# Optimization experiments

Measured on AMD Instinct MI355X. Metric: run time of the kernel, lower is better.

The kernel has to match this reference:

```python
import jax, jax.numpy as jnp
import numpy as np

N, E, H, NF, EF = 50000, 1600000, 128, 8, 2


def setup_inputs() -> dict:
    key = jax.random.key(0)
    ks = jax.random.split(key, 24)
    rn = lambda k, shp, s=0.05: jax.random.normal(k, shp, jnp.float32) * s
    inp = {
        "x": jax.random.normal(ks[0], (N, NF), jnp.float32),
        "edge_index": jax.random.randint(ks[1], (2, E), 0, N),
        "edge_attr": jax.random.normal(ks[2], (E, EF), jnp.float32),
        "enc_W": rn(ks[3], (NF, H)),
        "enc_b": jnp.zeros((H,), jnp.float32),
        "bn_g": jnp.ones((H,), jnp.float32),
        "bn_b": jnp.zeros((H,), jnp.float32),
    }
    i = 4
    for l in (1, 2, 3):
        inp[f"W{l}"] = rn(ks[i], (H, H))
        inp[f"asrc{l}"] = rn(ks[i + 1], (H,))
        inp[f"adst{l}"] = rn(ks[i + 2], (H,))
        inp[f"We{l}"] = rn(ks[i + 3], (EF, H))
        inp[f"ae{l}"] = rn(ks[i + 4], (H,))
        inp[f"b{l}"] = jnp.zeros((H,), jnp.float32)
        i += 5
    return inp


def _gat(h, src, dst, ea, W, a_s, a_d, We, a_e, b, n):
    # PyG GATConv, heads=1, concat=True, negative_slope=0.2
    g = h @ W                                   # [N, H] transformed nodes
    a_src = g @ a_s                             # [N] per-source attention term
    a_dst = g @ a_d                             # [N] per-target attention term
    a_edge = (ea @ We) @ a_e                    # [E'] edge-conditioned term
    logit = jax.nn.leaky_relu(a_src[src] + a_dst[dst] + a_edge, negative_slope=0.2)
    # scatter-softmax over incoming edges of each destination node
    m = jax.ops.segment_max(logit, dst, num_segments=n)
    e = jnp.exp(logit - m[dst])
    s = jax.ops.segment_sum(e, dst, num_segments=n)
    alpha = e / (s[dst] + 1e-16)                # [E']
    out = jax.ops.segment_sum(g[src] * alpha[:, None], dst, num_segments=n)
    return out + b


def _forward(x, edge_index, edge_attr, enc_W, enc_b, bn_g, bn_b,
             W1, asrc1, adst1, We1, ae1, b1,
             W2, asrc2, adst2, We2, ae2, b2,
             W3, asrc3, adst3, We3, ae3, b3):
    n = x.shape[0]
    # PyG add_self_loops=True with fill_value='mean' for edge_attr
    loop = jnp.arange(n)
    src = jnp.concatenate([edge_index[0], loop])
    dst = jnp.concatenate([edge_index[1], loop])
    ea = jnp.concatenate([edge_attr, jnp.broadcast_to(edge_attr.mean(0), (n, edge_attr.shape[1]))], axis=0)
    # node encoder: Linear -> BatchNorm1d (eval: running_mean=0, running_var=1) -> ReLU (dropout off)
    inv = np.float32(1.0 / np.sqrt(1.0 + 1e-5))
    h0 = jax.nn.relu((x @ enc_W + enc_b) * (bn_g * inv) + bn_b)
    h1 = jax.nn.relu(_gat(h0, src, dst, ea, W1, asrc1, adst1, We1, ae1, b1, n))
    h2 = jax.nn.relu(_gat(h1, src, dst, ea, W2, asrc2, adst2, We2, ae2, b2, n))
    h3 = _gat(h2, src, dst, ea, W3, asrc3, adst3, We3, ae3, b3, n)
    return h3 + h0


def reference(x, edge_index, edge_attr, enc_W, enc_b, bn_g, bn_b,
              W1, asrc1, adst1, We1, ae1, b1,
              W2, asrc2, adst2, We2, ae2, b2,
              W3, asrc3, adst3, We3, ae3, b3):
    return _forward(x, edge_index, edge_attr, enc_W, enc_b, bn_g, bn_b,
                    W1, asrc1, adst1, We1, ae1, b1,
                    W2, asrc2, adst2, We2, ae2, b2,
                    W3, asrc3, adst3, We3, ae3, b3)
```

## Files before the change

### kernel.cpp

```cpp
#include <hip/hip_runtime.h>
#include <math.h>


#define H 128
#define NF 8
#define EPB 4096

typedef __attribute__((ext_vector_type(8))) short short8v;
typedef __attribute__((ext_vector_type(4))) float f32x4;

__device__ __forceinline__ float wred_sum(float x) {
#pragma unroll
    for (int m = 32; m >= 1; m >>= 1) x += __shfl_xor(x, m, 64);
    return x;
}
__device__ __forceinline__ float wred_max(float x) {
#pragma unroll
    for (int m = 32; m >= 1; m >>= 1) x = fmaxf(x, __shfl_xor(x, m, 64));
    return x;
}
__device__ __forceinline__ ushort f2bf(float f) {
    uint u = __float_as_uint(f);
    uint r = (u + 0x7FFFu + ((u >> 16) & 1u)) >> 16;
    return (ushort)r;
}


__global__ void k_count(const int* __restrict__ ei, const float* __restrict__ ea,
                        int E, int nblk, int nbuckets, int* __restrict__ bucketTotal,
                        int* __restrict__ blockBase, float2* __restrict__ pmean) {
    __shared__ int hist[256];
    __shared__ float sx[4], sy[4];
    int t = threadIdx.x;
    int blk = blockIdx.x;
    hist[t] = 0;
    __syncthreads();
    int base = blk * EPB;
    float px = 0.f, py = 0.f;
#pragma unroll
    for (int i = 0; i < 16; ++i) {
        int e = base + i * 256 + t;
        if (e < E) {
            int d = ei[E + e];
            atomicAdd(&hist[d >> 8], 1);
            const float2 z = *(const float2*)(ea + 2 * (size_t)e);
            px += z.x; py += z.y;
        }
    }
    px = wred_sum(px); py = wred_sum(py);
    if ((t & 63) == 0) { sx[t >> 6] = px; sy[t >> 6] = py; }
    __syncthreads();
    if (t == 0) {
        pmean[blk] = make_float2(sx[0] + sx[1] + sx[2] + sx[3],
                                 sy[0] + sy[1] + sy[2] + sy[3]);
    }
    if (t < nbuckets) {
        int c = hist[t];
        int old = (c > 0) ? atomicAdd(&bucketTotal[t], c) : 0;
        blockBase[t * nblk + blk] = old;
    }
}

__global__ void k_scan_park(const int* __restrict__ bucketTotal, int nbuckets,
                            int* __restrict__ bucketBase, int* __restrict__ rowptr,
                            int N, int E, const float2* __restrict__ pmean, int nblk,
                            float invE,
                            const float* __restrict__ We1, const float* __restrict__ ae1,
                            const float* __restrict__ We2, const float* __restrict__ ae2,
                            const float* __restrict__ We3, const float* __restrict__ ae3,
                            float* __restrict__ park) {
    __shared__ int tmp[256];
    __shared__ float2 sp[4];
    __shared__ float smean[2];
    int t = threadIdx.x;
    float ax = 0.f, ay = 0.f;
    for (int i = t; i < nblk; i += 256) {
        float2 z = pmean[i];
        ax += z.x; ay += z.y;
    }
    ax = wred_sum(ax); ay = wred_sum(ay);
    if ((t & 63) == 0) sp[t >> 6] = make_float2(ax, ay);
    int v = (t < nbuckets) ? bucketTotal[t] : 0;
    tmp[t] = v;
    __syncthreads();
    for (int off = 1; off < 256; off <<= 1) {
        int q = (t >= off) ? tmp[t - off] : 0;
        __syncthreads();
        tmp[t] += q;
        __syncthreads();
    }
    bucketBase[t] = tmp[t] - v;
    if (t == 0) {
        bucketBase[256] = tmp[255];
        rowptr[N] = E;
        smean[0] = (sp[0].x + sp[1].x + sp[2].x + sp[3].x) * invE;
        smean[1] = (sp[0].y + sp[1].y + sp[2].y + sp[3].y) * invE;
    }
    __syncthreads();
    if (t < 192) {
        int l = t >> 6, q = t & 63;
        const float* We = (l == 0) ? We1 : ((l == 1) ? We2 : We3);
        const float* ae = (l == 0) ? ae1 : ((l == 1) ? ae2 : ae3);
        float p0 = We[q] * ae[q] + We[q + 64] * ae[q + 64];
        float p1 = We[H + q] * ae[q] + We[H + q + 64] * ae[q + 64];
        p0 = wred_sum(p0);
        p1 = wred_sum(p1);
        if (q == 0) {
            park[l * 3 + 0] = p0;
            park[l * 3 + 1] = p1;
            park[l * 3 + 2] = smean[0] * p0 + smean[1] * p1;
        }
    }
}

__global__ void k_place(const int* __restrict__ ei, const float* __restrict__ ea,
                        int E, int nblk, int nbuckets,
                        const int* __restrict__ bucketBase, const int* __restrict__ blockBase,
                        uint2* __restrict__ temp) {
    __shared__ int cnt[256];
    __shared__ int sbase[256];
    int t = threadIdx.x;
    int blk = blockIdx.x;
    cnt[t] = 0;
    if (t < nbuckets) sbase[t] = bucketBase[t] + blockBase[t * nblk + blk];
    __syncthreads();
    int base = blk * EPB;
#pragma unroll
    for (int i = 0; i < 16; ++i) {
        int e = base + i * 256 + t;
        if (e < E) {
            int s = ei[e];
            int d = ei[E + e];
            int b = d >> 8;
            int r = atomicAdd(&cnt[b], 1);
            const float2 z = *(const float2*)(ea + 2 * (size_t)e);
            uint w0 = (uint)s | ((uint)(d & 255) << 16);
            uint w1 = (uint)f2bf(z.x) | ((uint)f2bf(z.y) << 16);
            temp[sbase[b] + r] = make_uint2(w0, w1);
        }
    }
}

__global__ void k_fine(const uint2* __restrict__ temp, const int* __restrict__ bucketBase,
                       const float* __restrict__ park, int N,
                       uint* __restrict__ er0, uint* __restrict__ er1,
                       uint* __restrict__ er2, int* __restrict__ rowptr) {
    __shared__ int hist[256];
    __shared__ int tmp[256];
    __shared__ int fb[256];
    __shared__ int cur[256];
    int b = blockIdx.x;
    int t = threadIdx.x;
    const int lo = bucketBase[b], hi = bucketBase[b + 1];
    hist[t] = 0;
    __syncthreads();
    for (int e = lo + t; e < hi; e += 256) {
        atomicAdd(&hist[(temp[e].x >> 16) & 255], 1);
    }
    __syncthreads();
    int v = hist[t];
    tmp[t] = v;
    __syncthreads();
    for (int off = 1; off < 256; off <<= 1) {
        int q = (t >= off) ? tmp[t - off] : 0;
        __syncthreads();
        tmp[t] += q;
        __syncthreads();
    }
    fb[t] = tmp[t] - v;
    cur[t] = 0;
    int dst = b * 256 + t;
    if (dst < N) rowptr[dst] = lo + fb[t];
    __syncthreads();
    const float c00 = park[0], c01 = park[1];
    const float c10 = park[3], c11 = park[4];
    const float c20 = park[6], c21 = park[7];
    for (int e = lo + t; e < hi; e += 256) {
        uint2 w = temp[e];
        uint src = w.x & 0xFFFFu;
        int j = (int)((w.x >> 16) & 255u);
        float ex = __uint_as_float(w.y << 16);
        float ey = __uint_as_float(w.y & 0xffff0000u);
        int r = atomicAdd(&cur[j], 1);
        int p = lo + fb[j] + r;
        er0[p] = src | ((uint)f2bf(c00 * ex + c01 * ey) << 16);
        er1[p] = src | ((uint)f2bf(c10 * ex + c11 * ey) << 16);
        er2[p] = src | ((uint)f2bf(c20 * ex + c21 * ey) << 16);
    }
}

__global__ void k_wpack(const float* __restrict__ W1, const float* __restrict__ W2,
                        const float* __restrict__ W3, ushort* __restrict__ Wp) {
    int layer = blockIdx.x;
    const float* W = (layer == 0) ? W1 : ((layer == 1) ? W2 : W3);
    for (int idx = threadIdx.x; idx < 16384; idx += 256) {
        int i = idx & 7;
        int lane = (idx >> 3) & 63;
        int ft = idx >> 9;
        int kt = ft & 3, nt = ft >> 2;
        int k = kt * 32 + (lane >> 4) * 8 + i;
        int n = nt * 16 + (lane & 15);
        Wp[layer * 16384 + idx] = f2bf(W[k * H + n]);
    }
}

__global__ void k_encoder(const float* __restrict__ x, const float* __restrict__ encW,
                          const float* __restrict__ encb, const float* __restrict__ bng,
                          const float* __restrict__ bnb, float* __restrict__ h0,
                          ushort* __restrict__ hb, int N) {
    __shared__ float xs[8 * NF];
    int tid = threadIdx.x;
    int nb = blockIdx.x * 8;
    if (tid < 64) {
        size_t idx = (size_t)nb * NF + tid;
        xs[tid] = (idx < (size_t)N * NF) ? x[idx] : 0.f;
    }
    __syncthreads();
    int jt = tid & 31, i = tid >> 5;
    int node = nb + i;
    int j4 = jt * 4;
    float ax = 0.f, ay = 0.f, az = 0.f, aw = 0.f;
#pragma unroll
    for (int k = 0; k < NF; ++k) {
        float hx = xs[i * NF + k];
        const float4 w = *(const float4*)(encW + k * H + j4);
        ax = fmaf(hx, w.x, ax); ay = fmaf(hx, w.y, ay);
        az = fmaf(hx, w.z, az); aw = fmaf(hx, w.w, aw);
    }
    if (node < N) {
        const float inv = 0.9999950000374997f;
        const float4 eb = *(const float4*)(encb + j4);
        const float4 gg = *(const float4*)(bng + j4);
        const float4 bb = *(const float4*)(bnb + j4);
        float4 o;
        o.x = fmaxf(0.f, (ax + eb.x) * (gg.x * inv) + bb.x);
        o.y = fmaxf(0.f, (ay + eb.y) * (gg.y * inv) + bb.y);
        o.z = fmaxf(0.f, (az + eb.z) * (gg.z * inv) + bb.z);
        o.w = fmaxf(0.f, (aw + eb.w) * (gg.w * inv) + bb.w);
        *(float4*)(h0 + (size_t)node * H + j4) = o;
        uint2 ob;
        ob.x = (uint)f2bf(o.x) | ((uint)f2bf(o.y) << 16);
        ob.y = (uint)f2bf(o.z) | ((uint)f2bf(o.w) << 16);
        *(uint2*)(hb + (size_t)node * H + j4) = ob;
    }
}

__global__ void k_gemm_mfma(const ushort* __restrict__ hb, const ushort* __restrict__ Wp,
                            const float* __restrict__ avs, const float* __restrict__ avd,
                            ushort* __restrict__ gb, float* __restrict__ a_src,
                            float* __restrict__ a_dst, int N) {
    __shared__ ushort hs[64 * 136];
    int tid = threadIdx.x;
    int nb = blockIdx.x * 64;
#pragma unroll
    for (int it = 0; it < 4; ++it) {
        int fi = it * 256 + tid;
        int r = fi >> 4;
        int c8 = (fi & 15) * 8;
        int node = nb + r;
        uint4 v = make_uint4(0, 0, 0, 0);
        if (node < N) v = *(const uint4*)(hb + (size_t)node * H + c8);
        *(uint4*)(hs + r * 136 + c8) = v;
    }
    __syncthreads();
    const int l = tid & 63;
    const int w = tid >> 6;
    const int cl = l & 15;
    const int kg = l >> 4;
    const ushort* hrow = hs + (w * 16 + cl) * 136 + kg * 8;
    short8v a0 = *(const short8v*)(hrow + 0);
    short8v a1 = *(const short8v*)(hrow + 32);
    short8v a2 = *(const short8v*)(hrow + 64);
    short8v a3 = *(const short8v*)(hrow + 96);

    f32x4 acc[8];
#pragma unroll
    for (int nt = 0; nt < 8; ++nt) {
        const short8v* bp = (const short8v*)(Wp + ((size_t)(nt * 4) * 64 + l) * 8);
        f32x4 c = {0.f, 0.f, 0.f, 0.f};
        c = __builtin_amdgcn_mfma_f32_16x16x32_bf16(a0, bp[0], c, 0, 0, 0);
        c = __builtin_amdgcn_mfma_f32_16x16x32_bf16(a1, bp[64], c, 0, 0, 0);
        c = __builtin_amdgcn_mfma_f32_16x16x32_bf16(a2, bp[128], c, 0, 0, 0);
        c = __builtin_amdgcn_mfma_f32_16x16x32_bf16(a3, bp[192], c, 0, 0, 0);
        acc[nt] = c;
    }

    float ps0 = 0.f, ps1 = 0.f, ps2 = 0.f, ps3 = 0.f;
    float pd0 = 0.f, pd1 = 0.f, pd2 = 0.f, pd3 = 0.f;
#pragma unroll
    for (int nt = 0; nt < 8; ++nt) {
        float vs = avs[cl + 16 * nt];
        float vd = avd[cl + 16 * nt];
        ps0 = fmaf(acc[nt].x, vs, ps0); pd0 = fmaf(acc[nt].x, vd, pd0);
        ps1 = fmaf(acc[nt].y, vs, ps1); pd1 = fmaf(acc[nt].y, vd, pd1);
        ps2 = fmaf(acc[nt].z, vs, ps2); pd2 = fmaf(acc[nt].z, vd, pd2);
        ps3 = fmaf(acc[nt].w, vs, ps3); pd3 = fmaf(acc[nt].w, vd, pd3);
    }
#pragma unroll
    for (int m = 8; m >= 1; m >>= 1) {
        ps0 += __shfl_xor(ps0, m, 64); pd0 += __shfl_xor(pd0, m, 64);
        ps1 += __shfl_xor(ps1, m, 64); pd1 += __shfl_xor(pd1, m, 64);
        ps2 += __shfl_xor(ps2, m, 64); pd2 += __shfl_xor(pd2, m, 64);
        ps3 += __shfl_xor(ps3, m, 64); pd3 += __shfl_xor(pd3, m, 64);
    }
    int r0 = nb + w * 16 + kg * 4;
    if (cl == 0) {
        if (r0 + 0 < N) { a_src[r0 + 0] = ps0; a_dst[r0 + 0] = pd0; }
        if (r0 + 1 < N) { a_src[r0 + 1] = ps1; a_dst[r0 + 1] = pd1; }
        if (r0 + 2 < N) { a_src[r0 + 2] = ps2; a_dst[r0 + 2] = pd2; }
        if (r0 + 3 < N) { a_src[r0 + 3] = ps3; a_dst[r0 + 3] = pd3; }
    }
#pragma unroll
    for (int nt = 0; nt < 8; ++nt) {
        int col = nt * 16 + cl;
        if (r0 + 0 < N) gb[(size_t)(r0 + 0) * H + col] = f2bf(acc[nt].x);
        if (r0 + 1 < N) gb[(size_t)(r0 + 1) * H + col] = f2bf(acc[nt].y);
        if (r0 + 2 < N) gb[(size_t)(r0 + 2) * H + col] = f2bf(acc[nt].z);
        if (r0 + 3 < N) gb[(size_t)(r0 + 3) * H + col] = f2bf(acc[nt].w);
    }
}

template <int MODE>
__global__ void k_agg(const ushort* __restrict__ gb, const float* __restrict__ a_src,
                      const float* __restrict__ a_dst, const int* __restrict__ rowptr,
                      const uint* __restrict__ erecL, const float* __restrict__ park,
                      int layer, const float* __restrict__ bias,
                      const float* __restrict__ h0, float* __restrict__ outf,
                      ushort* __restrict__ outb, int N) {
    int wv = threadIdx.x >> 6;
    int lane = threadIdx.x & 63;
    int v = blockIdx.x * 4 + wv;
    if (v >= N) return;

    const int grp = lane >> 4;
    const int sub = lane & 15;
    const int ch8 = sub * 8;

    const float sa = park[layer * 3 + 2];
    const float adv = a_dst[v];
    float lself = a_src[v] + adv + sa;
    lself = (lself > 0.f) ? lself : 0.2f * lself;

    float m = lself;
    float s = 1.f;
    float acc[8];
    {
        const uint4 q = *(const uint4*)(gb + (size_t)v * H + ch8);
        float sel = (grp == 0) ? 1.f : 0.f;
        acc[0] = sel * __uint_as_float(q.x << 16);
        acc[1] = sel * __uint_as_float(q.x & 0xffff0000u);
        acc[2] = sel * __uint_as_float(q.y << 16);
        acc[3] = sel * __uint_as_float(q.y & 0xffff0000u);
        acc[4] = sel * __uint_as_float(q.z << 16);
        acc[5] = sel * __uint_as_float(q.z & 0xffff0000u);
        acc[6] = sel * __uint_as_float(q.w << 16);
        acc[7] = sel * __uint_as_float(q.w & 0xffff0000u);
    }

    const int rs = rowptr[v];
    const int re = rowptr[v + 1];
    for (int p0 = rs; p0 < re; p0 += 64) {
        int e = p0 + lane;
        bool val = e < re;
        uint rec = val ? erecL[e] : 0u;
        int sv = (int)(rec & 0xFFFFu);
        float lg;
        if (val) {
            float aef = __uint_as_float(rec & 0xffff0000u);
            lg = a_src[sv] + adv + aef;
            lg = (lg > 0.f) ? lg : 0.2f * lg;
        } else {
            lg = -INFINITY;
        }
        float cm = wred_max(lg);
        float nm = fmaxf(m, cm);
        float f = __expf(m - nm);
        float w = val ? __expf(lg - nm) : 0.f;
        float ws = wred_sum(w);
        s = s * f + ws;
#pragma unroll
        for (int k = 0; k < 8; ++k) acc[k] *= f;
        m = nm;

        int cnt = re - p0;
        if (cnt > 64) cnt = 64;
        const int cm1 = cnt - 1;
        const int iters = (cnt + 7) >> 3;

        int jA = grp, jB = grp + 4;
        int jAc = (jA <= cm1) ? jA : cm1;
        int jBc = (jB <= cm1) ? jB : cm1;
        float wA = __shfl(w, jAc, 64); if (jA > cm1) wA = 0.f;
        float wB = __shfl(w, jBc, 64); if (jB > cm1) wB = 0.f;
        int sA = __shfl(sv, jAc, 64);
        int sB = __shfl(sv, jBc, 64);
        uint4 qA = *(const uint4*)(gb + (size_t)sA * H + ch8);
        uint4 qB = *(const uint4*)(gb + (size_t)sB * H + ch8);

        for (int i = 0; i < iters; ++i) {
            int jA1 = (i + 1) * 8 + grp, jB1 = jA1 + 4;
            int jA1c = (jA1 <= cm1) ? jA1 : cm1;
            int jB1c = (jB1 <= cm1) ? jB1 : cm1;
            float wA1 = __shfl(w, jA1c, 64); if (jA1 > cm1) wA1 = 0.f;
            float wB1 = __shfl(w, jB1c, 64); if (jB1 > cm1) wB1 = 0.f;
            int sA1 = __shfl(sv, jA1c, 64);
            int sB1 = __shfl(sv, jB1c, 64);
            uint4 qA1 = *(const uint4*)(gb + (size_t)sA1 * H + ch8);
            uint4 qB1 = *(const uint4*)(gb + (size_t)sB1 * H + ch8);

            acc[0] = fmaf(wA, __uint_as_float(qA.x << 16), acc[0]);
            acc[1] = fmaf(wA, __uint_as_float(qA.x & 0xffff0000u), acc[1]);
            acc[2] = fmaf(wA, __uint_as_float(qA.y << 16), acc[2]);
            acc[3] = fmaf(wA, __uint_as_float(qA.y & 0xffff0000u), acc[3]);
            acc[4] = fmaf(wA, __uint_as_float(qA.z << 16), acc[4]);
            acc[5] = fmaf(wA, __uint_as_float(qA.z & 0xffff0000u), acc[5]);
            acc[6] = fmaf(wA, __uint_as_float(qA.w << 16), acc[6]);
            acc[7] = fmaf(wA, __uint_as_float(qA.w & 0xffff0000u), acc[7]);
            acc[0] = fmaf(wB, __uint_as_float(qB.x << 16), acc[0]);
            acc[1] = fmaf(wB, __uint_as_float(qB.x & 0xffff0000u), acc[1]);
            acc[2] = fmaf(wB, __uint_as_float(qB.y << 16), acc[2]);
            acc[3] = fmaf(wB, __uint_as_float(qB.y & 0xffff0000u), acc[3]);
            acc[4] = fmaf(wB, __uint_as_float(qB.z << 16), acc[4]);
            acc[5] = fmaf(wB, __uint_as_float(qB.z & 0xffff0000u), acc[5]);
            acc[6] = fmaf(wB, __uint_as_float(qB.w << 16), acc[6]);
            acc[7] = fmaf(wB, __uint_as_float(qB.w & 0xffff0000u), acc[7]);

            wA = wA1; wB = wB1; qA = qA1; qB = qB1;
        }
    }

#pragma unroll
    for (int k = 0; k < 8; ++k) {
        acc[k] += __shfl_xor(acc[k], 16, 64);
        acc[k] += __shfl_xor(acc[k], 32, 64);
    }

    if (grp == 0) {
        const float is = 1.f / s;
        const float4 b0 = *(const float4*)(bias + ch8);
        const float4 b1 = *(const float4*)(bias + ch8 + 4);
        float o[8];
        o[0] = acc[0] * is + b0.x; o[1] = acc[1] * is + b0.y;
        o[2] = acc[2] * is + b0.z; o[3] = acc[3] * is + b0.w;
        o[4] = acc[4] * is + b1.x; o[5] = acc[5] * is + b1.y;
        o[6] = acc[6] * is + b1.z; o[7] = acc[7] * is + b1.w;
        if (MODE == 0) {
#pragma unroll
            for (int k = 0; k < 8; ++k) o[k] = fmaxf(o[k], 0.f);
            uint4 ob;
            ob.x = (uint)f2bf(o[0]) | ((uint)f2bf(o[1]) << 16);
            ob.y = (uint)f2bf(o[2]) | ((uint)f2bf(o[3]) << 16);
            ob.z = (uint)f2bf(o[4]) | ((uint)f2bf(o[5]) << 16);
            ob.w = (uint)f2bf(o[6]) | ((uint)f2bf(o[7]) << 16);
            *(uint4*)(outb + (size_t)v * H + ch8) = ob;
        } else {
            const float4 ha = *(const float4*)(h0 + (size_t)v * H + ch8);
            const float4 hb4 = *(const float4*)(h0 + (size_t)v * H + ch8 + 4);
            o[0] += ha.x; o[1] += ha.y; o[2] += ha.z; o[3] += ha.w;
            o[4] += hb4.x; o[5] += hb4.y; o[6] += hb4.z; o[7] += hb4.w;
            *(float4*)(outf + (size_t)v * H + ch8) = make_float4(o[0], o[1], o[2], o[3]);
            *(float4*)(outf + (size_t)v * H + ch8 + 4) = make_float4(o[4], o[5], o[6], o[7]);
        }
    }
}


extern "C" void kernel_launch(void* const* d_in, const int* in_sizes, int n_in,
                              void* d_out, int out_size, void* d_ws, size_t ws_size,
                              hipStream_t stream) {
    const float* x    = (const float*)d_in[0];
    const int*   ei   = (const int*)d_in[1];
    const float* ea   = (const float*)d_in[2];
    const float* encW = (const float*)d_in[3];
    const float* encb = (const float*)d_in[4];
    const float* bng  = (const float*)d_in[5];
    const float* bnb  = (const float*)d_in[6];
    const float *W[3], *asrc[3], *adst[3], *We[3], *aev[3], *bias[3];
    for (int l = 0; l < 3; ++l) {
        W[l]    = (const float*)d_in[7 + l * 6 + 0];
        asrc[l] = (const float*)d_in[7 + l * 6 + 1];
        adst[l] = (const float*)d_in[7 + l * 6 + 2];
        We[l]   = (const float*)d_in[7 + l * 6 + 3];
        aev[l]  = (const float*)d_in[7 + l * 6 + 4];
        bias[l] = (const float*)d_in[7 + l * 6 + 5];
    }
    const int N = in_sizes[0] / NF;
    const int E = in_sizes[1] / 2;
    float* out = (float*)d_out;

    const int NBu  = (N + 255) >> 8;
    const int nblk = (E + EPB - 1) / EPB;

    char* wp = (char*)d_ws;
    auto alloc = [&](size_t bytes) -> char* {
        char* p = wp;
        wp += (bytes + 255) & ~(size_t)255;
        return p;
    };
    float*  h0       = (float*)alloc((size_t)N * H * 4);
    ushort* hb       = (ushort*)alloc((size_t)N * H * 2);
    ushort* gb       = (ushort*)alloc((size_t)N * H * 2);
    ushort* Wp       = (ushort*)alloc((size_t)3 * 16384 * 2);
    float*  a_src    = (float*)alloc((size_t)N * 4);
    float*  a_dst    = (float*)alloc((size_t)N * 4);
    int*    rowptr   = (int*)alloc((size_t)(N + 1) * 4);
    float*  park     = (float*)alloc(64);
    int*    bucketTotal = (int*)alloc(256 * 4);
    int*    bucketBase  = (int*)alloc(257 * 4);
    int*    blockBase   = (int*)alloc((size_t)NBu * nblk * 4);
    uint*   er0      = (uint*)alloc((size_t)E * 4);
    uint*   er1      = (uint*)alloc((size_t)E * 4);
    uint*   er2      = (uint*)alloc((size_t)E * 4);
    float2* pmean    = (float2*)alloc((size_t)nblk * 8);
    uint2*  temp     = (uint2*)h0;

    hipMemsetAsync(bucketTotal, 0, 256 * 4, stream);

    k_count<<<nblk, 256, 0, stream>>>(ei, ea, E, nblk, NBu, bucketTotal, blockBase, pmean);
    k_scan_park<<<1, 256, 0, stream>>>(bucketTotal, NBu, bucketBase, rowptr, N, E,
                                       pmean, nblk, 1.0f / (float)E,
                                       We[0], aev[0], We[1], aev[1], We[2], aev[2], park);
    k_place<<<nblk, 256, 0, stream>>>(ei, ea, E, nblk, NBu, bucketBase, blockBase, temp);
    k_fine<<<NBu, 256, 0, stream>>>(temp, bucketBase, park, N, er0, er1, er2, rowptr);
    k_wpack<<<3, 256, 0, stream>>>(W[0], W[1], W[2], Wp);

    const int GB8 = (N + 7) / 8;
    const int GBM = (N + 63) / 64;
    const int AB = (N + 3) / 4;
    k_encoder<<<GB8, 256, 0, stream>>>(x, encW, encb, bng, bnb, h0, hb, N);

    k_gemm_mfma<<<GBM, 256, 0, stream>>>(hb, Wp + 0 * 16384, asrc[0], adst[0],
                                         gb, a_src, a_dst, N);
    k_agg<0><<<AB, 256, 0, stream>>>(gb, a_src, a_dst, rowptr, er0, park, 0,
                                     bias[0], nullptr, nullptr, hb, N);
    k_gemm_mfma<<<GBM, 256, 0, stream>>>(hb, Wp + 1 * 16384, asrc[1], adst[1],
                                         gb, a_src, a_dst, N);
    k_agg<0><<<AB, 256, 0, stream>>>(gb, a_src, a_dst, rowptr, er1, park, 1,
                                     bias[1], nullptr, nullptr, hb, N);
    k_gemm_mfma<<<GBM, 256, 0, stream>>>(hb, Wp + 2 * 16384, asrc[2], adst[2],
                                         gb, a_src, a_dst, N);
    k_agg<1><<<AB, 256, 0, stream>>>(gb, a_src, a_dst, rowptr, er2, park, 2,
                                     bias[2], h0, out, nullptr, N);
}
```

Before: 313.1 us.

## Fuse CSR build stages with encoder, weight pack and first GEMM via block ranges

Independent preprocessing kernels are merged into two launches by giving each job its own block range. Edge counting runs alongside the node encoder and weight packing, and edge placement runs alongside the layer-1 MFMA GEMM. This removes launch gaps and lets independent work fill the GPU concurrently. The temp buffer now gets its own allocation instead of aliasing h0, which the encoder writes at the same time. The aggregation kernel also switches to packed float2 FMAs and nontemporal edge-record loads, at the cost of extra workspace memory and higher LDS use in the fused B blocks.

```diff
diff --git a/kernel.cpp b/kernel.cpp
--- a/kernel.cpp
+++ b/kernel.cpp
@@ -8,6 +8,7 @@
 
 typedef __attribute__((ext_vector_type(8))) short short8v;
 typedef __attribute__((ext_vector_type(4))) float f32x4;
+typedef __attribute__((ext_vector_type(2))) float f32x2;
 
 __device__ __forceinline__ float wred_sum(float x) {
 #pragma unroll
@@ -24,40 +25,102 @@
     uint r = (u + 0x7FFFu + ((u >> 16) & 1u)) >> 16;
     return (ushort)r;
 }
-
-
-__global__ void k_count(const int* __restrict__ ei, const float* __restrict__ ea,
-                        int E, int nblk, int nbuckets, int* __restrict__ bucketTotal,
-                        int* __restrict__ blockBase, float2* __restrict__ pmean) {
+__device__ __forceinline__ f32x2 bfpair(uint q) {
+    f32x2 r;
+    r.x = __uint_as_float(q << 16);
+    r.y = __uint_as_float(q & 0xffff0000u);
+    return r;
+}
+
+__global__ void k_fusedA(const int* __restrict__ ei, const float* __restrict__ ea,
+                         int E, int nblk, int nbuckets, int* __restrict__ bucketTotal,
+                         int* __restrict__ blockBase, float2* __restrict__ pmean,
+                         const float* __restrict__ x, const float* __restrict__ encW,
+                         const float* __restrict__ encb, const float* __restrict__ bng,
+                         const float* __restrict__ bnb, float* __restrict__ h0,
+                         ushort* __restrict__ hb, int N, int GB8,
+                         const float* __restrict__ W1, const float* __restrict__ W2,
+                         const float* __restrict__ W3, ushort* __restrict__ Wp) {
     __shared__ int hist[256];
     __shared__ float sx[4], sy[4];
-    int t = threadIdx.x;
-    int blk = blockIdx.x;
-    hist[t] = 0;
-    __syncthreads();
-    int base = blk * EPB;
-    float px = 0.f, py = 0.f;
-#pragma unroll
-    for (int i = 0; i < 16; ++i) {
-        int e = base + i * 256 + t;
-        if (e < E) {
-            int d = ei[E + e];
-            atomicAdd(&hist[d >> 8], 1);
-            const float2 z = *(const float2*)(ea + 2 * (size_t)e);
-            px += z.x; py += z.y;
-        }
-    }
-    px = wred_sum(px); py = wred_sum(py);
-    if ((t & 63) == 0) { sx[t >> 6] = px; sy[t >> 6] = py; }
-    __syncthreads();
-    if (t == 0) {
-        pmean[blk] = make_float2(sx[0] + sx[1] + sx[2] + sx[3],
-                                 sy[0] + sy[1] + sy[2] + sy[3]);
-    }
-    if (t < nbuckets) {
-        int c = hist[t];
-        int old = (c > 0) ? atomicAdd(&bucketTotal[t], c) : 0;
-        blockBase[t * nblk + blk] = old;
+    __shared__ float xs[8 * NF];
+    const int bx = blockIdx.x;
+    const int t = threadIdx.x;
+
+    if (bx < nblk) {
+        int blk = bx;
+        hist[t] = 0;
+        __syncthreads();
+        int base = blk * EPB;
+        float px = 0.f, py = 0.f;
+#pragma unroll
+        for (int i = 0; i < 16; ++i) {
+            int e = base + i * 256 + t;
+            if (e < E) {
+                int d = ei[E + e];
+                atomicAdd(&hist[d >> 8], 1);
+                const float2 z = *(const float2*)(ea + 2 * (size_t)e);
+                px += z.x; py += z.y;
+            }
+        }
+        px = wred_sum(px); py = wred_sum(py);
+        if ((t & 63) == 0) { sx[t >> 6] = px; sy[t >> 6] = py; }
+        __syncthreads();
+        if (t == 0) {
+            pmean[blk] = make_float2(sx[0] + sx[1] + sx[2] + sx[3],
+                                     sy[0] + sy[1] + sy[2] + sy[3]);
+        }
+        if (t < nbuckets) {
+            int c = hist[t];
+            int old = (c > 0) ? atomicAdd(&bucketTotal[t], c) : 0;
+            blockBase[t * nblk + blk] = old;
+        }
+    } else if (bx < nblk + GB8) {
+        int nb = (bx - nblk) * 8;
+        if (t < 64) {
+            size_t idx = (size_t)nb * NF + t;
+            xs[t] = (idx < (size_t)N * NF) ? x[idx] : 0.f;
+        }
+        __syncthreads();
+        int jt = t & 31, i = t >> 5;
+        int node = nb + i;
+        int j4 = jt * 4;
+        float ax = 0.f, ay = 0.f, az = 0.f, aw = 0.f;
+#pragma unroll
+        for (int k = 0; k < NF; ++k) {
+            float hx = xs[i * NF + k];
+            const float4 w = *(const float4*)(encW + k * H + j4);
+            ax = fmaf(hx, w.x, ax); ay = fmaf(hx, w.y, ay);
+            az = fmaf(hx, w.z, az); aw = fmaf(hx, w.w, aw);
+        }
+        if (node < N) {
+            const float inv = 0.9999950000374997f;
+            const float4 eb = *(const float4*)(encb + j4);
+            const float4 gg = *(const float4*)(bng + j4);
+            const float4 bb = *(const float4*)(bnb + j4);
+            float4 o;
+            o.x = fmaxf(0.f, (ax + eb.x) * (gg.x * inv) + bb.x);
+            o.y = fmaxf(0.f, (ay + eb.y) * (gg.y * inv) + bb.y);
+            o.z = fmaxf(0.f, (az + eb.z) * (gg.z * inv) + bb.z);
+            o.w = fmaxf(0.f, (aw + eb.w) * (gg.w * inv) + bb.w);
+            *(float4*)(h0 + (size_t)node * H + j4) = o;
+            uint2 ob;
+            ob.x = (uint)f2bf(o.x) | ((uint)f2bf(o.y) << 16);
+            ob.y = (uint)f2bf(o.z) | ((uint)f2bf(o.w) << 16);
+            *(uint2*)(hb + (size_t)node * H + j4) = ob;
+        }
+    } else {
+        int layer = bx - nblk - GB8;
+        const float* W = (layer == 0) ? W1 : ((layer == 1) ? W2 : W3);
+        for (int idx = t; idx < 16384; idx += 256) {
+            int i = idx & 7;
+            int lane = (idx >> 3) & 63;
+            int ft = idx >> 9;
+            int kt = ft & 3, nt = ft >> 2;
+            int k = kt * 32 + (lane >> 4) * 8 + i;
+            int n = nt * 16 + (lane & 15);
+            Wp[layer * 16384 + idx] = f2bf(W[k * H + n]);
+        }
     }
 }
 
@@ -113,31 +176,108 @@
     }
 }
 
-__global__ void k_place(const int* __restrict__ ei, const float* __restrict__ ea,
-                        int E, int nblk, int nbuckets,
-                        const int* __restrict__ bucketBase, const int* __restrict__ blockBase,
-                        uint2* __restrict__ temp) {
+__global__ void k_fusedB(const int* __restrict__ ei, const float* __restrict__ ea,
+                         int E, int nblk, int nbuckets,
+                         const int* __restrict__ bucketBase, const int* __restrict__ blockBase,
+                         uint2* __restrict__ temp,
+                         const ushort* __restrict__ hb, const ushort* __restrict__ Wp,
+                         const float* __restrict__ avs, const float* __restrict__ avd,
+                         ushort* __restrict__ gb, float* __restrict__ a_src,
+                         float* __restrict__ a_dst, int N) {
     __shared__ int cnt[256];
     __shared__ int sbase[256];
-    int t = threadIdx.x;
-    int blk = blockIdx.x;
-    cnt[t] = 0;
-    if (t < nbuckets) sbase[t] = bucketBase[t] + blockBase[t * nblk + blk];
-    __syncthreads();
-    int base = blk * EPB;
-#pragma unroll
-    for (int i = 0; i < 16; ++i) {
-        int e = base + i * 256 + t;
-        if (e < E) {
-            int s = ei[e];
-            int d = ei[E + e];
-            int b = d >> 8;
-            int r = atomicAdd(&cnt[b], 1);
-            const float2 z = *(const float2*)(ea + 2 * (size_t)e);
-            uint w0 = (uint)s | ((uint)(d & 255) << 16);
-            uint w1 = (uint)f2bf(z.x) | ((uint)f2bf(z.y) << 16);
-            temp[sbase[b] + r] = make_uint2(w0, w1);
-        }
+    __shared__ ushort hs[64 * 136];
+    const int tid = threadIdx.x;
+
+    if (blockIdx.x < nblk) {
+        int blk = blockIdx.x;
+        cnt[tid] = 0;
+        if (tid < nbuckets) sbase[tid] = bucketBase[tid] + blockBase[tid * nblk + blk];
+        __syncthreads();
+        int base = blk * EPB;
+#pragma unroll
+        for (int i = 0; i < 16; ++i) {
+            int e = base + i * 256 + tid;
+            if (e < E) {
+                int s = ei[e];
+                int d = ei[E + e];
+                int b = d >> 8;
+                int r = atomicAdd(&cnt[b], 1);
+                const float2 z = *(const float2*)(ea + 2 * (size_t)e);
+                uint w0 = (uint)s | ((uint)(d & 255) << 16);
+                uint w1 = (uint)f2bf(z.x) | ((uint)f2bf(z.y) << 16);
+                temp[sbase[b] + r] = make_uint2(w0, w1);
+            }
+        }
+        return;
+    }
+
+    int nb = (blockIdx.x - nblk) * 64;
+#pragma unroll
+    for (int it = 0; it < 4; ++it) {
+        int fi = it * 256 + tid;
+        int r = fi >> 4;
+        int c8 = (fi & 15) * 8;
+        int node = nb + r;
+        uint4 v = make_uint4(0, 0, 0, 0);
+        if (node < N) v = *(const uint4*)(hb + (size_t)node * H + c8);
+        *(uint4*)(hs + r * 136 + c8) = v;
+    }
+    __syncthreads();
+    const int l = tid & 63;
+    const int w = tid >> 6;
+    const int cl = l & 15;
+    const int kg = l >> 4;
+    const ushort* hrow = hs + (w * 16 + cl) * 136 + kg * 8;
+    short8v a0 = *(const short8v*)(hrow + 0);
+    short8v a1 = *(const short8v*)(hrow + 32);
+    short8v a2 = *(const short8v*)(hrow + 64);
+    short8v a3 = *(const short8v*)(hrow + 96);
+
+    f32x4 acc[8];
+#pragma unroll
+    for (int nt = 0; nt < 8; ++nt) {
+        const short8v* bp = (const short8v*)(Wp + ((size_t)(nt * 4) * 64 + l) * 8);
+        f32x4 c = {0.f, 0.f, 0.f, 0.f};
+        c = __builtin_amdgcn_mfma_f32_16x16x32_bf16(a0, bp[0], c, 0, 0, 0);
+        c = __builtin_amdgcn_mfma_f32_16x16x32_bf16(a1, bp[64], c, 0, 0, 0);
+        c = __builtin_amdgcn_mfma_f32_16x16x32_bf16(a2, bp[128], c, 0, 0, 0);
+        c = __builtin_amdgcn_mfma_f32_16x16x32_bf16(a3, bp[192], c, 0, 0, 0);
+        acc[nt] = c;
+    }
+
+    float ps0 = 0.f, ps1 = 0.f, ps2 = 0.f, ps3 = 0.f;
+    float pd0 = 0.f, pd1 = 0.f, pd2 = 0.f, pd3 = 0.f;
+#pragma unroll
+    for (int nt = 0; nt < 8; ++nt) {
+        float vs = avs[cl + 16 * nt];
+        float vd = avd[cl + 16 * nt];
+        ps0 = fmaf(acc[nt].x, vs, ps0); pd0 = fmaf(acc[nt].x, vd, pd0);
+        ps1 = fmaf(acc[nt].y, vs, ps1); pd1 = fmaf(acc[nt].y, vd, pd1);
+        ps2 = fmaf(acc[nt].z, vs, ps2); pd2 = fmaf(acc[nt].z, vd, pd2);
+        ps3 = fmaf(acc[nt].w, vs, ps3); pd3 = fmaf(acc[nt].w, vd, pd3);
+    }
+#pragma unroll
+    for (int m = 8; m >= 1; m >>= 1) {
+        ps0 += __shfl_xor(ps0, m, 64); pd0 += __shfl_xor(pd0, m, 64);
+        ps1 += __shfl_xor(ps1, m, 64); pd1 += __shfl_xor(pd1, m, 64);
+        ps2 += __shfl_xor(ps2, m, 64); pd2 += __shfl_xor(pd2, m, 64);
+        ps3 += __shfl_xor(ps3, m, 64); pd3 += __shfl_xor(pd3, m, 64);
+    }
+    int r0 = nb + w * 16 + kg * 4;
+    if (cl == 0) {
+        if (r0 + 0 < N) { a_src[r0 + 0] = ps0; a_dst[r0 + 0] = pd0; }
+        if (r0 + 1 < N) { a_src[r0 + 1] = ps1; a_dst[r0 + 1] = pd1; }
+        if (r0 + 2 < N) { a_src[r0 + 2] = ps2; a_dst[r0 + 2] = pd2; }
+        if (r0 + 3 < N) { a_src[r0 + 3] = ps3; a_dst[r0 + 3] = pd3; }
+    }
+#pragma unroll
+    for (int nt = 0; nt < 8; ++nt) {
+        int col = nt * 16 + cl;
+        if (r0 + 0 < N) gb[(size_t)(r0 + 0) * H + col] = f2bf(acc[nt].x);
+        if (r0 + 1 < N) gb[(size_t)(r0 + 1) * H + col] = f2bf(acc[nt].y);
+        if (r0 + 2 < N) gb[(size_t)(r0 + 2) * H + col] = f2bf(acc[nt].z);
+        if (r0 + 3 < N) gb[(size_t)(r0 + 3) * H + col] = f2bf(acc[nt].w);
     }
 }
 
@@ -189,62 +329,6 @@
     }
 }
 
-__global__ void k_wpack(const float* __restrict__ W1, const float* __restrict__ W2,
-                        const float* __restrict__ W3, ushort* __restrict__ Wp) {
-    int layer = blockIdx.x;
-    const float* W = (layer == 0) ? W1 : ((layer == 1) ? W2 : W3);
-    for (int idx = threadIdx.x; idx < 16384; idx += 256) {
-        int i = idx & 7;
-        int lane = (idx >> 3) & 63;
-        int ft = idx >> 9;
-        int kt = ft & 3, nt = ft >> 2;
-        int k = kt * 32 + (lane >> 4) * 8 + i;
-        int n = nt * 16 + (lane & 15);
-        Wp[layer * 16384 + idx] = f2bf(W[k * H + n]);
-    }
-}
-
-__global__ void k_encoder(const float* __restrict__ x, const float* __restrict__ encW,
-                          const float* __restrict__ encb, const float* __restrict__ bng,
-                          const float* __restrict__ bnb, float* __restrict__ h0,
-                          ushort* __restrict__ hb, int N) {
-    __shared__ float xs[8 * NF];
-    int tid = threadIdx.x;
-    int nb = blockIdx.x * 8;
-    if (tid < 64) {
-        size_t idx = (size_t)nb * NF + tid;
-        xs[tid] = (idx < (size_t)N * NF) ? x[idx] : 0.f;
-    }
-    __syncthreads();
-    int jt = tid & 31, i = tid >> 5;
-    int node = nb + i;
-    int j4 = jt * 4;
-    float ax = 0.f, ay = 0.f, az = 0.f, aw = 0.f;
-#pragma unroll
-    for (int k = 0; k < NF; ++k) {
-        float hx = xs[i * NF + k];
-        const float4 w = *(const float4*)(encW + k * H + j4);
-        ax = fmaf(hx, w.x, ax); ay = fmaf(hx, w.y, ay);
-        az = fmaf(hx, w.z, az); aw = fmaf(hx, w.w, aw);
-    }
-    if (node < N) {
-        const float inv = 0.9999950000374997f;
-        const float4 eb = *(const float4*)(encb + j4);
-        const float4 gg = *(const float4*)(bng + j4);
-        const float4 bb = *(const float4*)(bnb + j4);
-        float4 o;
-        o.x = fmaxf(0.f, (ax + eb.x) * (gg.x * inv) + bb.x);
-        o.y = fmaxf(0.f, (ay + eb.y) * (gg.y * inv) + bb.y);
-        o.z = fmaxf(0.f, (az + eb.z) * (gg.z * inv) + bb.z);
-        o.w = fmaxf(0.f, (aw + eb.w) * (gg.w * inv) + bb.w);
-        *(float4*)(h0 + (size_t)node * H + j4) = o;
-        uint2 ob;
-        ob.x = (uint)f2bf(o.x) | ((uint)f2bf(o.y) << 16);
-        ob.y = (uint)f2bf(o.z) | ((uint)f2bf(o.w) << 16);
-        *(uint2*)(hb + (size_t)node * H + j4) = ob;
-    }
-}
-
 __global__ void k_gemm_mfma(const ushort* __restrict__ hb, const ushort* __restrict__ Wp,
                             const float* __restrict__ avs, const float* __restrict__ avd,
                             ushort* __restrict__ gb, float* __restrict__ a_src,
@@ -343,18 +427,14 @@
 
     float m = lself;
     float s = 1.f;
-    float acc[8];
+    f32x2 acc2[4];
     {
         const uint4 q = *(const uint4*)(gb + (size_t)v * H + ch8);
         float sel = (grp == 0) ? 1.f : 0.f;
-        acc[0] = sel * __uint_as_float(q.x << 16);
-        acc[1] = sel * __uint_as_float(q.x & 0xffff0000u);
-        acc[2] = sel * __uint_as_float(q.y << 16);
-        acc[3] = sel * __uint_as_float(q.y & 0xffff0000u);
-        acc[4] = sel * __uint_as_float(q.z << 16);
-        acc[5] = sel * __uint_as_float(q.z & 0xffff0000u);
-        acc[6] = sel * __uint_as_float(q.w << 16);
-        acc[7] = sel * __uint_as_float(q.w & 0xffff0000u);
+        acc2[0] = bfpair(q.x) * sel;
+        acc2[1] = bfpair(q.y) * sel;
+        acc2[2] = bfpair(q.z) * sel;
+        acc2[3] = bfpair(q.w) * sel;
     }
 
     const int rs = rowptr[v];
@@ -362,7 +442,7 @@
     for (int p0 = rs; p0 < re; p0 += 64) {
         int e = p0 + lane;
         bool val = e < re;
-        uint rec = val ? erecL[e] : 0u;
+        uint rec = val ? __builtin_nontemporal_load(erecL + e) : 0u;
         int sv = (int)(rec & 0xFFFFu);
         float lg;
         if (val) {
@@ -379,7 +459,7 @@
         float ws = wred_sum(w);
         s = s * f + ws;
 #pragma unroll
-        for (int k = 0; k < 8; ++k) acc[k] *= f;
+        for (int k = 0; k < 4; ++k) acc2[k] *= f;
         m = nm;
 
         int cnt = re - p0;
@@ -408,27 +488,26 @@
             uint4 qA1 = *(const uint4*)(gb + (size_t)sA1 * H + ch8);
             uint4 qB1 = *(const uint4*)(gb + (size_t)sB1 * H + ch8);
 
-            acc[0] = fmaf(wA, __uint_as_float(qA.x << 16), acc[0]);
-            acc[1] = fmaf(wA, __uint_as_float(qA.x & 0xffff0000u), acc[1]);
-            acc[2] = fmaf(wA, __uint_as_float(qA.y << 16), acc[2]);
-            acc[3] = fmaf(wA, __uint_as_float(qA.y & 0xffff0000u), acc[3]);
-            acc[4] = fmaf(wA, __uint_as_float(qA.z << 16), acc[4]);
-            acc[5] = fmaf(wA, __uint_as_float(qA.z & 0xffff0000u), acc[5]);
-            acc[6] = fmaf(wA, __uint_as_float(qA.w << 16), acc[6]);
-            acc[7] = fmaf(wA, __uint_as_float(qA.w & 0xffff0000u), acc[7]);
-            acc[0] = fmaf(wB, __uint_as_float(qB.x << 16), acc[0]);
-            acc[1] = fmaf(wB, __uint_as_float(qB.x & 0xffff0000u), acc[1]);
-            acc[2] = fmaf(wB, __uint_as_float(qB.y << 16), acc[2]);
-            acc[3] = fmaf(wB, __uint_as_float(qB.y & 0xffff0000u), acc[3]);
-            acc[4] = fmaf(wB, __uint_as_float(qB.z << 16), acc[4]);
-            acc[5] = fmaf(wB, __uint_as_float(qB.z & 0xffff0000u), acc[5]);
-            acc[6] = fmaf(wB, __uint_as_float(qB.w << 16), acc[6]);
-            acc[7] = fmaf(wB, __uint_as_float(qB.w & 0xffff0000u), acc[7]);
+            f32x2 wAv = {wA, wA};
+            f32x2 wBv = {wB, wB};
+            acc2[0] = __builtin_elementwise_fma(wAv, bfpair(qA.x), acc2[0]);
+            acc2[1] = __builtin_elementwise_fma(wAv, bfpair(qA.y), acc2[1]);
+            acc2[2] = __builtin_elementwise_fma(wAv, bfpair(qA.z), acc2[2]);
+            acc2[3] = __builtin_elementwise_fma(wAv, bfpair(qA.w), acc2[3]);
+            acc2[0] = __builtin_elementwise_fma(wBv, bfpair(qB.x), acc2[0]);
+            acc2[1] = __builtin_elementwise_fma(wBv, bfpair(qB.y), acc2[1]);
+            acc2[2] = __builtin_elementwise_fma(wBv, bfpair(qB.z), acc2[2]);
+            acc2[3] = __builtin_elementwise_fma(wBv, bfpair(qB.w), acc2[3]);
 
             wA = wA1; wB = wB1; qA = qA1; qB = qB1;
         }
     }
 
+    float acc[8];
+    acc[0] = acc2[0].x; acc[1] = acc2[0].y;
+    acc[2] = acc2[1].x; acc[3] = acc2[1].y;
+    acc[4] = acc2[2].x; acc[5] = acc2[2].y;
+    acc[6] = acc2[3].x; acc[7] = acc2[3].y;
 #pragma unroll
     for (int k = 0; k < 8; ++k) {
         acc[k] += __shfl_xor(acc[k], 16, 64);
@@ -490,6 +569,9 @@
 
     const int NBu  = (N + 255) >> 8;
     const int nblk = (E + EPB - 1) / EPB;
+    const int GB8  = (N + 7) / 8;
+    const int GBM  = (N + 63) / 64;
+    const int AB   = (N + 3) / 4;
 
     char* wp = (char*)d_ws;
     auto alloc = [&](size_t bytes) -> char* {
@@ -512,25 +594,22 @@
     uint*   er1      = (uint*)alloc((size_t)E * 4);
     uint*   er2      = (uint*)alloc((size_t)E * 4);
     float2* pmean    = (float2*)alloc((size_t)nblk * 8);
-    uint2*  temp     = (uint2*)h0;
+    uint2*  temp     = (uint2*)alloc((size_t)E * 8);
 
     hipMemsetAsync(bucketTotal, 0, 256 * 4, stream);
 
-    k_count<<<nblk, 256, 0, stream>>>(ei, ea, E, nblk, NBu, bucketTotal, blockBase, pmean);
+    k_fusedA<<<nblk + GB8 + 3, 256, 0, stream>>>(
+        ei, ea, E, nblk, NBu, bucketTotal, blockBase, pmean,
+        x, encW, encb, bng, bnb, h0, hb, N, GB8,
+        W[0], W[1], W[2], Wp);
     k_scan_park<<<1, 256, 0, stream>>>(bucketTotal, NBu, bucketBase, rowptr, N, E,
                                        pmean, nblk, 1.0f / (float)E,
                                        We[0], aev[0], We[1], aev[1], We[2], aev[2], park);
-    k_place<<<nblk, 256, 0, stream>>>(ei, ea, E, nblk, NBu, bucketBase, blockBase, temp);
+    k_fusedB<<<nblk + GBM, 256, 0, stream>>>(
+        ei, ea, E, nblk, NBu, bucketBase, blockBase, temp,
+        hb, Wp + 0 * 16384, asrc[0], adst[0], gb, a_src, a_dst, N);
     k_fine<<<NBu, 256, 0, stream>>>(temp, bucketBase, park, N, er0, er1, er2, rowptr);
-    k_wpack<<<3, 256, 0, stream>>>(W[0], W[1], W[2], Wp);
-
-    const int GB8 = (N + 7) / 8;
-    const int GBM = (N + 63) / 64;
-    const int AB = (N + 3) / 4;
-    k_encoder<<<GB8, 256, 0, stream>>>(x, encW, encb, bng, bnb, h0, hb, N);
-
-    k_gemm_mfma<<<GBM, 256, 0, stream>>>(hb, Wp + 0 * 16384, asrc[0], adst[0],
-                                         gb, a_src, a_dst, N);
+
     k_agg<0><<<AB, 256, 0, stream>>>(gb, a_src, a_dst, rowptr, er0, park, 0,
                                      bias[0], nullptr, nullptr, hb, N);
     k_gemm_mfma<<<GBM, 256, 0, stream>>>(hb, Wp + 1 * 16384, asrc[1], adst[1],
```

Measured after the change: 298.8 us. -4.6%, faster.
